# Optimization experiments

Measured on AMD Instinct MI355X. Metric: run time of the kernel, lower is better.

## Reference

```python
import jax, jax.numpy as jnp
import numpy as np

N = 20000
E = 320000
H = 16
C = 16
NUM_GRAPHS = 64
NEG_SLOPE = 0.2


def _gat(x, edge_index, W, a_src, a_dst, bias):
    # PyG GATConv, concat=True, shared lin for src/dst, eval mode (no dropout)
    h = (x @ W).reshape(-1, H, C)                       # [N,H,C]
    src, dst = edge_index[0], edge_index[1]
    alpha_src = jnp.sum(h * a_src, axis=-1)             # [N,H]
    alpha_dst = jnp.sum(h * a_dst, axis=-1)             # [N,H]
    alpha = alpha_src[src] + alpha_dst[dst]             # [E,H]
    alpha = jax.nn.leaky_relu(alpha, NEG_SLOPE)
    amax = jax.ops.segment_max(alpha, dst, num_segments=N)
    ex = jnp.exp(alpha - amax[dst])
    denom = jax.ops.segment_sum(ex, dst, num_segments=N)
    attn = ex / jnp.where(denom == 0, 1.0, denom)[dst]  # [E,H]
    msg = h[src] * attn[:, :, None]                     # [E,H,C]
    out = jax.ops.segment_sum(msg, dst, num_segments=N) # [N,H,C]
    return out.reshape(-1, H * C) + bias


def setup_inputs() -> dict:
    key = jax.random.key(0)
    ks = jax.random.split(key, 32)
    d = {}
    d['x'] = jax.random.normal(ks[0], (N, 20), dtype=jnp.float32)
    d['edge_index_ipv6'] = jax.random.randint(ks[1], (2, E), 0, N)
    d['edge_attr_ipv6'] = jax.random.normal(ks[2], (E, 19), dtype=jnp.float32)
    d['edge_index_tsch'] = jax.random.randint(ks[3], (2, E), 0, N)
    d['edge_attr_tsch'] = jax.random.normal(ks[4], (E, 7), dtype=jnp.float32)
    d['batch'] = jnp.sort(jax.random.randint(ks[5], (N,), 0, NUM_GRAPHS))
    s = 0.1
    d['W_i'] = jax.random.normal(ks[6], (20, H * C), dtype=jnp.float32) * s
    d['a_src_i'] = jax.random.normal(ks[7], (H, C), dtype=jnp.float32) * s
    d['a_dst_i'] = jax.random.normal(ks[8], (H, C), dtype=jnp.float32) * s
    d['b_i'] = jnp.zeros((H * C,), dtype=jnp.float32)
    d['W_t'] = jax.random.normal(ks[9], (20, H * C), dtype=jnp.float32) * s
    d['a_src_t'] = jax.random.normal(ks[10], (H, C), dtype=jnp.float32) * s
    d['a_dst_t'] = jax.random.normal(ks[11], (H, C), dtype=jnp.float32) * s
    d['b_t'] = jnp.zeros((H * C,), dtype=jnp.float32)
    d['Wf'] = jax.random.normal(ks[12], (512, 64), dtype=jnp.float32) * s
    d['bf'] = jnp.zeros((64,), dtype=jnp.float32)
    d['W1'] = jax.random.normal(ks[13], (64, 32), dtype=jnp.float32) * s
    d['b1'] = jnp.zeros((32,), dtype=jnp.float32)
    d['W2'] = jax.random.normal(ks[14], (32, 16), dtype=jnp.float32) * s
    d['b2'] = jnp.zeros((16,), dtype=jnp.float32)
    d['W3'] = jax.random.normal(ks[15], (16, 16), dtype=jnp.float32) * s
    d['b3'] = jnp.zeros((16,), dtype=jnp.float32)
    d['Wce'] = jax.random.normal(ks[16], (16, 3), dtype=jnp.float32) * s
    d['bce'] = jnp.zeros((3,), dtype=jnp.float32)
    d['Wcv'] = jax.random.normal(ks[17], (16, 3), dtype=jnp.float32) * s
    d['bcv'] = jnp.zeros((3,), dtype=jnp.float32)
    return d


def reference(x, edge_index_ipv6, edge_attr_ipv6, edge_index_tsch, edge_attr_tsch,
              batch, W_i, a_src_i, a_dst_i, b_i, W_t, a_src_t, a_dst_t, b_t,
              Wf, bf, W1, b1, W2, b2, W3, b3, Wce, bce, Wcv, bcv):
    # edge_attr_* are ignored by GATConv (edge_dim=None in PyG), as in original
    n_ipv6 = _gat(x, edge_index_ipv6, W_i, a_src_i, a_dst_i, b_i)
    n_tsch = _gat(x, edge_index_tsch, W_t, a_src_t, a_dst_t, b_t)
    h = jnp.concatenate([n_ipv6, n_tsch], axis=-1)      # [N,512]
    h = jax.nn.relu(h @ Wf + bf)
    h = jax.nn.relu(h @ W1 + b1)
    h = jax.nn.relu(h @ W2 + b2)
    h = jax.nn.relu(h @ W3 + b3)                        # [N,16]
    ssum = jax.ops.segment_sum(h, batch, num_segments=NUM_GRAPHS)
    cnt = jax.ops.segment_sum(jnp.ones((h.shape[0], 1), h.dtype), batch,
                              num_segments=NUM_GRAPHS)
    g = ssum / jnp.where(cnt == 0, 1.0, cnt)            # [G,16]
    out_event = g @ Wce + bce
    out_env = g @ Wcv + bcv
    return out_event, out_env
```

## Files before the change

### kernel.cpp

```cpp
#include <hip/hip_runtime.h>
#include <math.h>

#define N_NODES 20000
#define N_EDGES 320000
#define NG 64
#define NEG 0.2f
#define NCHUNK ((N_NODES + 255) / 256)
#define FLAGBIT (1 << 30)

typedef __attribute__((ext_vector_type(8))) short bf16x8;
typedef __attribute__((ext_vector_type(4))) float f32x4;

__device__ __forceinline__ unsigned short f2bf(float f) {
  unsigned int u = __float_as_uint(f);
  return (unsigned short)((u + 0x7fffu + ((u >> 16) & 1u)) >> 16);
}
__device__ __forceinline__ unsigned int pk2bf(float a, float b) {
  return (unsigned int)f2bf(a) | ((unsigned int)f2bf(b) << 16);
}

__global__ __launch_bounds__(256) void k_prep(
    const float* __restrict__ W_i, const float* __restrict__ as_i, const float* __restrict__ ad_i,
    const float* __restrict__ W_t, const float* __restrict__ as_t, const float* __restrict__ ad_t,
    const float* __restrict__ Wf, const float* __restrict__ bf,
    const float* __restrict__ b_i, const float* __restrict__ b_t,
    float* __restrict__ wsall, unsigned short* __restrict__ wbigfrag,
    float* __restrict__ bfold,
    int* __restrict__ fill_i, int* __restrict__ fill_t,
    float* __restrict__ gsum, int* __restrict__ gcnt, int* __restrict__ aggs) {
  __shared__ float bred[4][64];
  int idx = blockIdx.x * 256 + threadIdx.x;
  if (idx < 1280) {
    int k = idx >> 6, c = idx & 63;
    int set = c >> 5, role = (c >> 4) & 1, h = c & 15;
    const float* W = set ? W_t : W_i;
    const float* a = set ? (role ? ad_t : as_t) : (role ? ad_i : as_i);
    float v = 0.f;
#pragma unroll
    for (int j = 0; j < 16; ++j) v = fmaf(W[k * 256 + h * 16 + j], a[h * 16 + j], v);
    wsall[idx] = v;
    return;
  }
  idx -= 1280;
  if (idx < 40960) {
    int ct = idx / 10240, rem = idx % 10240;
    int lane = (rem >> 3) & 63, j = rem & 7, ks = rem >> 9;
    int k = ks * 32 + ((lane >> 4) << 3) + j;
    int nc = ct * 16 + (lane & 15);
    int g = (k >= 320) ? 1 : 0;
    int r = k - g * 320;
    int ch = r >> 4, h = r & 15;
    float v = 0.f;
    if (ch < 20) {
      const float* W = g ? W_t : W_i;
      const float* wr = W + ch * 256 + (h << 4);
      const float* wf = Wf + ((g << 8) + (h << 4)) * 64 + nc;
#pragma unroll
      for (int m = 0; m < 16; ++m) v = fmaf(wr[m], wf[m * 64], v);
    }
    wbigfrag[idx] = f2bf(v);
    return;
  }
  idx -= 40960;
  if (idx < 256) {
    int t = threadIdx.x, wv = t >> 6, j = t & 63;
    float p = 0.f;
    int i0 = wv * 128;
#pragma unroll 4
    for (int i = i0; i < i0 + 128; ++i) {
      float b = (i < 256) ? b_i[i] : b_t[i - 256];
      p = fmaf(b, Wf[i * 64 + j], p);
    }
    bred[wv][j] = p;
    __syncthreads();
    if (wv == 0) bfold[j] = bred[0][j] + bred[1][j] + bred[2][j] + bred[3][j] + bf[j];
    return;
  }
  idx -= 256;
  if (idx < N_NODES) { fill_i[idx] = 0; return; }
  idx -= N_NODES;
  if (idx < N_NODES) { fill_t[idx] = 0; return; }
  idx -= N_NODES;
  if (idx < NG * 16) { gsum[idx] = 0.f; return; }
  idx -= NG * 16;
  if (idx < NG) { gcnt[idx] = 0; return; }
  idx -= NG;
  if (idx < 256) aggs[idx] = 0;
}

__global__ __launch_bounds__(256) void k_alpha(
    const float* __restrict__ x, const float* __restrict__ wsall,
    unsigned short* __restrict__ xpadbf,
    float* __restrict__ asrc0, float* __restrict__ adst0,
    float* __restrict__ asrc1, float* __restrict__ adst1) {
  int t = threadIdx.x;
  int n0 = blockIdx.x * 16;
  __shared__ float xs[16][20];
  __shared__ float ws[20][64];
  for (int i = t; i < 16 * 20; i += 256) {
    int nd = i / 20, k = i % 20;
    xs[nd][k] = x[(n0 + nd) * 20 + k];
  }
  for (int i = t; i < 1280; i += 256) ws[i >> 6][i & 63] = wsall[i];
  __syncthreads();
  for (int i = t; i < 512; i += 256) {
    int nd = i >> 5, j = i & 31;
    float v = (j < 20) ? xs[nd][j] : (j == 20 ? 1.f : 0.f);
    xpadbf[(size_t)(n0 + nd) * 32 + j] = f2bf(v);
  }
#pragma unroll
  for (int i = 0; i < 4; ++i) {
    int wi = i * 256 + t;
    int nd = wi >> 6, c = wi & 63;
    float v = 0.f;
#pragma unroll
    for (int k = 0; k < 20; ++k) v = fmaf(xs[nd][k], ws[k][c], v);
    int n = n0 + nd, h = c & 15;
    float* arr = (c >> 5) ? ((c >> 4) & 1 ? adst1 : asrc1)
                          : ((c >> 4) & 1 ? adst0 : asrc0);
    arr[n * 16 + h] = v;
  }
}

__global__ void k_hist(const int* __restrict__ ei0, const int* __restrict__ ei1,
                       int* __restrict__ cnt0, int* __restrict__ cnt1) {
  int e = blockIdx.x * blockDim.x + threadIdx.x;
  if (e >= N_EDGES) return;
  if (blockIdx.y == 0)
    atomicAdd(&cnt0[ei0[N_EDGES + e]], 1);
  else
    atomicAdd(&cnt1[ei1[N_EDGES + e]], 1);
}

__global__ __launch_bounds__(256) void k_scan(
    int* __restrict__ fill0, int* __restrict__ fill1,
    int* __restrict__ rp0, int* __restrict__ rp1,
    int* __restrict__ aggs) {
  int chunk = blockIdx.x, set = blockIdx.y;
  int* fill = set ? fill1 : fill0;
  int* rp = set ? rp1 : rp0;
  int t = threadIdx.x, lane = t & 63, wv = t >> 6;
  int i = chunk * 256 + t;
  int v = (i < N_NODES) ? fill[i] : 0;
  int s = v;
#pragma unroll
  for (int d = 1; d < 64; d <<= 1) {
    int o = __shfl_up(s, d);
    if (lane >= d) s += o;
  }
  __shared__ int wsum[4];
  if (lane == 63) wsum[wv] = s;
  __syncthreads();
  int pre = 0;
#pragma unroll
  for (int j = 0; j < 4; ++j)
    if (j < wv) pre += wsum[j];
  s += pre;
  int agg = wsum[0] + wsum[1] + wsum[2] + wsum[3];
  if (t == 0)
    __hip_atomic_store(&aggs[set * 128 + chunk], agg | FLAGBIT,
                       __ATOMIC_RELEASE, __HIP_MEMORY_SCOPE_AGENT);
  __shared__ int reds[256];
  int part = 0;
  for (int j = t; j < chunk; j += 256) {
    int a;
    do {
      a = __hip_atomic_load(&aggs[set * 128 + j], __ATOMIC_ACQUIRE,
                            __HIP_MEMORY_SCOPE_AGENT);
    } while (!(a & FLAGBIT));
    part += a & (FLAGBIT - 1);
  }
  reds[t] = part;
  __syncthreads();
  for (int st = 128; st > 0; st >>= 1) {
    if (t < st) reds[t] += reds[t + st];
    __syncthreads();
  }
  int carry = reds[0];
  int excl = carry + s - v;
  if (i < N_NODES) {
    rp[i] = excl;
    fill[i] = excl;
    if (i == N_NODES - 1) rp[N_NODES] = excl + v;
  }
}

__global__ void k_scatter(const int* __restrict__ ei0, const int* __restrict__ ei1,
                          int* __restrict__ fill0, int* __restrict__ fill1,
                          unsigned short* __restrict__ srcs0,
                          unsigned short* __restrict__ srcs1) {
  int e = blockIdx.x * blockDim.x + threadIdx.x;
  if (e >= N_EDGES) return;
  const int* ei = blockIdx.y ? ei1 : ei0;
  int* fill = blockIdx.y ? fill1 : fill0;
  unsigned short* srcs = blockIdx.y ? srcs1 : srcs0;
  int d = ei[N_EDGES + e];
  int pos = atomicAdd(&fill[d], 1);
  srcs[pos] = (unsigned short)ei[e];
}

__global__ __launch_bounds__(256) void k_gat(
    const unsigned short* __restrict__ xpadbf,
    const float* __restrict__ asrc0, const float* __restrict__ adst0,
    const float* __restrict__ asrc1, const float* __restrict__ adst1,
    const int* __restrict__ rp0, const unsigned short* __restrict__ srcs0,
    const int* __restrict__ rp1, const unsigned short* __restrict__ srcs1,
    unsigned short* __restrict__ xagg) {
  __shared__ unsigned short exsh[4][16][40];
  __shared__ unsigned short xtsh[4][2][16][40];
  int w4 = threadIdx.x >> 6, lane = threadIdx.x & 63;
  int n = blockIdx.x * 2 + (w4 >> 1);
  int g = w4 & 1;
  int eid = lane & 15, slot = lane >> 4;
  unsigned short (*ext)[40] = exsh[w4];
  unsigned short (*xtw)[16][40] = xtsh[w4];
  const float* asrc = g ? asrc1 : asrc0;
  const float* adst = g ? adst1 : adst0;
  const int* rp = g ? rp1 : rp0;
  const unsigned short* srcs = g ? srcs1 : srcs0;
  int k0 = rp[n], k1 = rp[n + 1];
  const float4 adn4 = *(const float4*)&adst[n * 16 + slot * 4];
  f32x4 acc0 = {0.f, 0.f, 0.f, 0.f}, acc1 = acc0;
  int h16 = lane & 15, e8 = (lane >> 4) * 8;
  for (int base = k0; base < k1; base += 32) {
    int e0 = base + 2 * eid, e1 = e0 + 1;
    int sa = (int)srcs[min(e0, k1 - 1)];
    int sbb = (int)srcs[min(e1, k1 - 1)];
    const float4 ava = *(const float4*)&asrc[sa * 16 + slot * 4];
    const float4 avb = *(const float4*)&asrc[sbb * 16 + slot * 4];
    const uint4 xra = *(const uint4*)&xpadbf[(size_t)sa * 32 + slot * 8];
    const uint4 xrb = *(const uint4*)&xpadbf[(size_t)sbb * 32 + slot * 8];
    float ea[4], eb[4];
    {
      float a;
      bool v0 = e0 < k1, v1 = e1 < k1;
      a = ava.x + adn4.x; a = a >= 0.f ? a : NEG * a; ea[0] = v0 ? __expf(a) : 0.f;
      a = ava.y + adn4.y; a = a >= 0.f ? a : NEG * a; ea[1] = v0 ? __expf(a) : 0.f;
      a = ava.z + adn4.z; a = a >= 0.f ? a : NEG * a; ea[2] = v0 ? __expf(a) : 0.f;
      a = ava.w + adn4.w; a = a >= 0.f ? a : NEG * a; ea[3] = v0 ? __expf(a) : 0.f;
      a = avb.x + adn4.x; a = a >= 0.f ? a : NEG * a; eb[0] = v1 ? __expf(a) : 0.f;
      a = avb.y + adn4.y; a = a >= 0.f ? a : NEG * a; eb[1] = v1 ? __expf(a) : 0.f;
      a = avb.z + adn4.z; a = a >= 0.f ? a : NEG * a; eb[2] = v1 ? __expf(a) : 0.f;
      a = avb.w + adn4.w; a = a >= 0.f ? a : NEG * a; eb[3] = v1 ? __expf(a) : 0.f;
    }
#pragma unroll
    for (int r = 0; r < 4; ++r)
      *(unsigned int*)&ext[slot * 4 + r][2 * eid] = pk2bf(ea[r], eb[r]);
    unsigned int ua[4] = {xra.x, xra.y, xra.z, xra.w};
    unsigned int ub[4] = {xrb.x, xrb.y, xrb.z, xrb.w};
#pragma unroll
    for (int q = 0; q < 8; ++q) {
      unsigned int baq = (q & 1) ? (ua[q >> 1] >> 16) : (ua[q >> 1] & 0xffffu);
      unsigned int bbq = (q & 1) ? (ub[q >> 1] >> 16) : (ub[q >> 1] & 0xffffu);
      int ch = slot * 8 + q;
      *(unsigned int*)&xtw[ch >> 4][ch & 15][2 * eid] = baq | (bbq << 16);
    }
    bf16x8 A = *(const bf16x8*)&ext[h16][e8];
    bf16x8 B0 = *(const bf16x8*)&xtw[0][h16][e8];
    bf16x8 B1 = *(const bf16x8*)&xtw[1][h16][e8];
    acc0 = __builtin_amdgcn_mfma_f32_16x16x32_bf16(A, B0, acc0, 0, 0, 0);
    acc1 = __builtin_amdgcn_mfma_f32_16x16x32_bf16(A, B1, acc1, 0, 0, 0);
  }
  float inv[4];
#pragma unroll
  for (int r = 0; r < 4; ++r) {
    float dr = __shfl(acc1[r], (lane & 48) | 4);
    inv[r] = dr > 0.f ? 1.f / dr : 0.f;
  }
  int s = lane >> 4, c = lane & 15;
  size_t nb = (size_t)n * 640 + g * 320;
  uint2 o0;
  o0.x = pk2bf(acc0[0] * inv[0], acc0[1] * inv[1]);
  o0.y = pk2bf(acc0[2] * inv[2], acc0[3] * inv[3]);
  *(uint2*)&xagg[nb + c * 16 + s * 4] = o0;
  if (c < 4) {
    uint2 o1;
    o1.x = pk2bf(acc1[0] * inv[0], acc1[1] * inv[1]);
    o1.y = pk2bf(acc1[2] * inv[2], acc1[3] * inv[3]);
    *(uint2*)&xagg[nb + 256 + c * 16 + s * 4] = o1;
  }
}

__global__ __launch_bounds__(256) void k_mlp(
    const unsigned short* __restrict__ xagg, const unsigned short* __restrict__ wbigfrag,
    const float* __restrict__ bfold,
    const float* __restrict__ W1m, const float* __restrict__ b1v,
    const float* __restrict__ W2m, const float* __restrict__ b2v,
    const float* __restrict__ W3m, const float* __restrict__ b3v,
    const int* __restrict__ batch,
    float* __restrict__ gsum, int* __restrict__ gcnt) {
  int t = threadIdx.x, w = t >> 6, lane = t & 63;
  int n0 = blockIdx.x * 16;
  __shared__ float o1[16][68];
  __shared__ float o2[16][36];
  __shared__ float o3[16][20];
  __shared__ float o4[16][17];
  __shared__ int bs[16];
  if (t < 16) bs[t] = batch[n0 + t];

  {
    int m = lane & 15, kb = lane >> 4;
    const unsigned short* aptr = xagg + (size_t)(n0 + m) * 640 + kb * 8;
    const unsigned short* bbase = wbigfrag + (size_t)w * 10240 + lane * 8;
    f32x4 acc = {0.f, 0.f, 0.f, 0.f};
#pragma unroll 5
    for (int ks = 0; ks < 20; ++ks) {
      bf16x8 af = *(const bf16x8*)(aptr + ks * 32);
      bf16x8 bfr = *(const bf16x8*)(bbase + (size_t)ks * 512);
      acc = __builtin_amdgcn_mfma_f32_16x16x32_bf16(af, bfr, acc, 0, 0, 0);
    }
    int col = lane & 15, rg = lane >> 4;
#pragma unroll
    for (int r = 0; r < 4; ++r) {
      int row = rg * 4 + r;
      o1[row][w * 16 + col] = fmaxf(acc[r] + bfold[w * 16 + col], 0.f);
    }
  }
  __syncthreads();
  int nd = t >> 4, js = t & 15;
  {
    float a0 = b1v[js], a1 = b1v[js + 16];
#pragma unroll 8
    for (int k = 0; k < 64; ++k) {
      float hv = o1[nd][k];
      a0 = fmaf(hv, W1m[k * 32 + js], a0);
      a1 = fmaf(hv, W1m[k * 32 + js + 16], a1);
    }
    o2[nd][js] = fmaxf(a0, 0.f);
    o2[nd][js + 16] = fmaxf(a1, 0.f);
  }
  __syncthreads();
  {
    float a = b2v[js];
#pragma unroll
    for (int k = 0; k < 32; ++k) a = fmaf(o2[nd][k], W2m[k * 16 + js], a);
    o3[nd][js] = fmaxf(a, 0.f);
  }
  __syncthreads();
  {
    float a = b3v[js];
#pragma unroll
    for (int k = 0; k < 16; ++k) a = fmaf(o3[nd][k], W3m[k * 16 + js], a);
    o4[nd][js] = fmaxf(a, 0.f);
  }
  __syncthreads();
  if (t < 128) {
    int s = t >> 4, jx = t & 15;
    int b = bs[0] + s;
    if (b <= bs[15]) {
      float sum = 0.f; int c = 0;
#pragma unroll
      for (int ndd = 0; ndd < 16; ++ndd)
        if (bs[ndd] == b) { sum += o4[ndd][jx]; ++c; }
      if (c > 0) {
        atomicAdd(&gsum[b * 16 + jx], sum);
        if (jx == 0) atomicAdd(&gcnt[b], c);
      }
    }
  }
}

__global__ void k_head(const float* __restrict__ gsum, const int* __restrict__ gcnt,
                       const float* __restrict__ Wce, const float* __restrict__ bce,
                       const float* __restrict__ Wcv, const float* __restrict__ bcv,
                       float* __restrict__ out) {
  int t = threadIdx.x;
  if (t >= 384) return;
  int half = t / 192, idx = t % 192;
  int b = idx / 3, r = idx % 3;
  float cnt = (float)gcnt[b];
  float inv = cnt > 0.f ? 1.f / cnt : 1.f;
  const float* Wc = half ? Wcv : Wce;
  const float* bc = half ? bcv : bce;
  float v = bc[r];
#pragma unroll
  for (int j = 0; j < 16; ++j) v = fmaf(gsum[b * 16 + j] * inv, Wc[j * 3 + r], v);
  out[t] = v;
}

extern "C" void kernel_launch(void* const* d_in, const int* in_sizes, int n_in,
                              void* d_out, int out_size, void* d_ws, size_t ws_size,
                              hipStream_t stream) {
  const float* x = (const float*)d_in[0];
  const int* ei_i = (const int*)d_in[1];
  const int* ei_t = (const int*)d_in[3];
  const int* batch = (const int*)d_in[5];
  const float* W_i = (const float*)d_in[6];
  const float* as_i = (const float*)d_in[7];
  const float* ad_i = (const float*)d_in[8];
  const float* b_i = (const float*)d_in[9];
  const float* W_t = (const float*)d_in[10];
  const float* as_t = (const float*)d_in[11];
  const float* ad_t = (const float*)d_in[12];
  const float* b_t = (const float*)d_in[13];
  const float* Wf = (const float*)d_in[14];
  const float* bf = (const float*)d_in[15];
  const float* W1 = (const float*)d_in[16];
  const float* b1 = (const float*)d_in[17];
  const float* W2 = (const float*)d_in[18];
  const float* b2 = (const float*)d_in[19];
  const float* W3 = (const float*)d_in[20];
  const float* b3 = (const float*)d_in[21];
  const float* Wce = (const float*)d_in[22];
  const float* bce = (const float*)d_in[23];
  const float* Wcv = (const float*)d_in[24];
  const float* bcv = (const float*)d_in[25];

  char* ws = (char*)d_ws;
  size_t off = 0;
  auto take = [&](size_t bytes) {
    void* p = ws + off;
    off = (off + bytes + 255) & ~(size_t)255;
    return p;
  };
  unsigned short* xpadbf = (unsigned short*)take((size_t)N_NODES * 32 * 2);
  unsigned short* xagg = (unsigned short*)take((size_t)N_NODES * 640 * 2);
  float* wsall = (float*)take((size_t)1280 * 4);
  unsigned short* wbigfrag = (unsigned short*)take((size_t)40960 * 2);
  float* bfold = (float*)take((size_t)64 * 4);
  float* asrc_i = (float*)take((size_t)N_NODES * 16 * 4);
  float* adst_i = (float*)take((size_t)N_NODES * 16 * 4);
  float* asrc_t = (float*)take((size_t)N_NODES * 16 * 4);
  float* adst_t = (float*)take((size_t)N_NODES * 16 * 4);
  int* rowptr_i = (int*)take((size_t)(N_NODES + 1) * 4);
  int* rowptr_t = (int*)take((size_t)(N_NODES + 1) * 4);
  int* fill_i = (int*)take((size_t)N_NODES * 4);
  int* fill_t = (int*)take((size_t)N_NODES * 4);
  int* csums = (int*)take((size_t)2 * 128 * 4);
  unsigned short* srcs_i = (unsigned short*)take((size_t)N_EDGES * 2);
  unsigned short* srcs_t = (unsigned short*)take((size_t)N_EDGES * 2);
  float* gsum = (float*)take((size_t)NG * 16 * 4);
  int* gcnt = (int*)take((size_t)NG * 4);

  int prep_items = 1280 + 40960 + 256 + N_NODES + N_NODES + NG * 16 + NG + 256;
  k_prep<<<(prep_items + 255) / 256, 256, 0, stream>>>(
      W_i, as_i, ad_i, W_t, as_t, ad_t, Wf, bf, b_i, b_t,
      wsall, wbigfrag, bfold, fill_i, fill_t, gsum, gcnt, csums);

  k_alpha<<<N_NODES / 16, 256, 0, stream>>>(x, wsall, xpadbf,
                                            asrc_i, adst_i, asrc_t, adst_t);

  dim3 egrid((N_EDGES + 255) / 256, 2);
  k_hist<<<egrid, 256, 0, stream>>>(ei_i, ei_t, fill_i, fill_t);
  dim3 sgrid(NCHUNK, 2);
  k_scan<<<sgrid, 256, 0, stream>>>(fill_i, fill_t, rowptr_i, rowptr_t, csums);
  k_scatter<<<egrid, 256, 0, stream>>>(ei_i, ei_t, fill_i, fill_t, srcs_i, srcs_t);

  k_gat<<<N_NODES / 2, 256, 0, stream>>>(xpadbf, asrc_i, adst_i, asrc_t, adst_t,
                                         rowptr_i, srcs_i, rowptr_t, srcs_t,
                                         xagg);

  k_mlp<<<N_NODES / 16, 256, 0, stream>>>(xagg, wbigfrag, bfold,
                                          W1, b1, W2, b2, W3, b3,
                                          batch, gsum, gcnt);

  k_head<<<1, 384, 0, stream>>>(gsum, gcnt, Wce, bce, Wcv, bcv, (float*)d_out);
}
```

Baseline: 136.8 us.

## Fuse prep, alpha and histogram kernels into one front kernel; zero buffers via memset

Merges the weight-prep, per-node attention-logit, and in-degree histogram kernels into a single launch. Each node-block now recomputes the folded W·a weights in shared memory instead of reading a precomputed buffer, and also handles 256 edges of the histogram for both graphs. Buffer zeroing moves to two hipMemsetAsync calls over contiguous allocations. The aim is fewer launches and fewer inter-kernel dependencies, at the cost of redundant weight folding in every block and memsets that still serialize on the stream.

```diff
diff --git a/kernel.cpp b/kernel.cpp
--- a/kernel.cpp
+++ b/kernel.cpp
@@ -19,30 +19,24 @@
   return (unsigned int)f2bf(a) | ((unsigned int)f2bf(b) << 16);
 }
 
-__global__ __launch_bounds__(256) void k_prep(
+__global__ __launch_bounds__(256) void k_front(
+    const float* __restrict__ x,
     const float* __restrict__ W_i, const float* __restrict__ as_i, const float* __restrict__ ad_i,
     const float* __restrict__ W_t, const float* __restrict__ as_t, const float* __restrict__ ad_t,
     const float* __restrict__ Wf, const float* __restrict__ bf,
     const float* __restrict__ b_i, const float* __restrict__ b_t,
-    float* __restrict__ wsall, unsigned short* __restrict__ wbigfrag,
-    float* __restrict__ bfold,
-    int* __restrict__ fill_i, int* __restrict__ fill_t,
-    float* __restrict__ gsum, int* __restrict__ gcnt, int* __restrict__ aggs) {
+    const int* __restrict__ ei0, const int* __restrict__ ei1,
+    unsigned short* __restrict__ wbigfrag, float* __restrict__ bfold,
+    unsigned short* __restrict__ xpadbf,
+    float* __restrict__ asrc0, float* __restrict__ adst0,
+    float* __restrict__ asrc1, float* __restrict__ adst1,
+    int* __restrict__ fill0, int* __restrict__ fill1) {
   __shared__ float bred[4][64];
-  int idx = blockIdx.x * 256 + threadIdx.x;
-  if (idx < 1280) {
-    int k = idx >> 6, c = idx & 63;
-    int set = c >> 5, role = (c >> 4) & 1, h = c & 15;
-    const float* W = set ? W_t : W_i;
-    const float* a = set ? (role ? ad_t : as_t) : (role ? ad_i : as_i);
-    float v = 0.f;
-#pragma unroll
-    for (int j = 0; j < 16; ++j) v = fmaf(W[k * 256 + h * 16 + j], a[h * 16 + j], v);
-    wsall[idx] = v;
-    return;
-  }
-  idx -= 1280;
-  if (idx < 40960) {
+  __shared__ float xs[16][20];
+  __shared__ float ws[20][64];
+  int b = blockIdx.x, t = threadIdx.x;
+  if (b < 160) {
+    int idx = b * 256 + t;
     int ct = idx / 10240, rem = idx % 10240;
     int lane = (rem >> 3) & 63, j = rem & 7, ks = rem >> 9;
     int k = ks * 32 + ((lane >> 4) << 3) + j;
@@ -61,47 +55,41 @@
     wbigfrag[idx] = f2bf(v);
     return;
   }
-  idx -= 40960;
-  if (idx < 256) {
-    int t = threadIdx.x, wv = t >> 6, j = t & 63;
+  if (b == 160) {
+    int wv = t >> 6, j = t & 63;
     float p = 0.f;
     int i0 = wv * 128;
 #pragma unroll 4
     for (int i = i0; i < i0 + 128; ++i) {
-      float b = (i < 256) ? b_i[i] : b_t[i - 256];
-      p = fmaf(b, Wf[i * 64 + j], p);
+      float bb = (i < 256) ? b_i[i] : b_t[i - 256];
+      p = fmaf(bb, Wf[i * 64 + j], p);
     }
     bred[wv][j] = p;
     __syncthreads();
     if (wv == 0) bfold[j] = bred[0][j] + bred[1][j] + bred[2][j] + bred[3][j] + bf[j];
     return;
   }
-  idx -= 256;
-  if (idx < N_NODES) { fill_i[idx] = 0; return; }
-  idx -= N_NODES;
-  if (idx < N_NODES) { fill_t[idx] = 0; return; }
-  idx -= N_NODES;
-  if (idx < NG * 16) { gsum[idx] = 0.f; return; }
-  idx -= NG * 16;
-  if (idx < NG) { gcnt[idx] = 0; return; }
-  idx -= NG;
-  if (idx < 256) aggs[idx] = 0;
-}
-
-__global__ __launch_bounds__(256) void k_alpha(
-    const float* __restrict__ x, const float* __restrict__ wsall,
-    unsigned short* __restrict__ xpadbf,
-    float* __restrict__ asrc0, float* __restrict__ adst0,
-    float* __restrict__ asrc1, float* __restrict__ adst1) {
-  int t = threadIdx.x;
-  int n0 = blockIdx.x * 16;
-  __shared__ float xs[16][20];
-  __shared__ float ws[20][64];
-  for (int i = t; i < 16 * 20; i += 256) {
+  int a = b - 161;
+  int e = a * 256 + t;
+  int d0 = ei0[N_EDGES + e];
+  int d1 = ei1[N_EDGES + e];
+  atomicAdd(&fill0[d0], 1);
+  atomicAdd(&fill1[d1], 1);
+  int n0 = a * 16;
+  for (int i = t; i < 320; i += 256) {
     int nd = i / 20, k = i % 20;
     xs[nd][k] = x[(n0 + nd) * 20 + k];
   }
-  for (int i = t; i < 1280; i += 256) ws[i >> 6][i & 63] = wsall[i];
+  for (int i = t; i < 1280; i += 256) {
+    int k = i >> 6, c = i & 63;
+    int set = c >> 5, role = (c >> 4) & 1, h = c & 15;
+    const float* W = set ? W_t : W_i;
+    const float* av = set ? (role ? ad_t : as_t) : (role ? ad_i : as_i);
+    float v = 0.f;
+#pragma unroll
+    for (int j = 0; j < 16; ++j) v = fmaf(W[k * 256 + h * 16 + j], av[h * 16 + j], v);
+    ws[k][c] = v;
+  }
   __syncthreads();
   for (int i = t; i < 512; i += 256) {
     int nd = i >> 5, j = i & 31;
@@ -120,16 +108,6 @@
                           : ((c >> 4) & 1 ? adst0 : asrc0);
     arr[n * 16 + h] = v;
   }
-}
-
-__global__ void k_hist(const int* __restrict__ ei0, const int* __restrict__ ei1,
-                       int* __restrict__ cnt0, int* __restrict__ cnt1) {
-  int e = blockIdx.x * blockDim.x + threadIdx.x;
-  if (e >= N_EDGES) return;
-  if (blockIdx.y == 0)
-    atomicAdd(&cnt0[ei0[N_EDGES + e]], 1);
-  else
-    atomicAdd(&cnt1[ei1[N_EDGES + e]], 1);
 }
 
 __global__ __launch_bounds__(256) void k_scan(
@@ -415,7 +393,6 @@
   };
   unsigned short* xpadbf = (unsigned short*)take((size_t)N_NODES * 32 * 2);
   unsigned short* xagg = (unsigned short*)take((size_t)N_NODES * 640 * 2);
-  float* wsall = (float*)take((size_t)1280 * 4);
   unsigned short* wbigfrag = (unsigned short*)take((size_t)40960 * 2);
   float* bfold = (float*)take((size_t)64 * 4);
   float* asrc_i = (float*)take((size_t)N_NODES * 16 * 4);
@@ -424,26 +401,27 @@
   float* adst_t = (float*)take((size_t)N_NODES * 16 * 4);
   int* rowptr_i = (int*)take((size_t)(N_NODES + 1) * 4);
   int* rowptr_t = (int*)take((size_t)(N_NODES + 1) * 4);
-  int* fill_i = (int*)take((size_t)N_NODES * 4);
-  int* fill_t = (int*)take((size_t)N_NODES * 4);
-  int* csums = (int*)take((size_t)2 * 128 * 4);
+  int* fill_i = (int*)take((size_t)2 * N_NODES * 4);
+  int* fill_t = fill_i + N_NODES;
   unsigned short* srcs_i = (unsigned short*)take((size_t)N_EDGES * 2);
   unsigned short* srcs_t = (unsigned short*)take((size_t)N_EDGES * 2);
-  float* gsum = (float*)take((size_t)NG * 16 * 4);
-  int* gcnt = (int*)take((size_t)NG * 4);
-
-  int prep_items = 1280 + 40960 + 256 + N_NODES + N_NODES + NG * 16 + NG + 256;
-  k_prep<<<(prep_items + 255) / 256, 256, 0, stream>>>(
-      W_i, as_i, ad_i, W_t, as_t, ad_t, Wf, bf, b_i, b_t,
-      wsall, wbigfrag, bfold, fill_i, fill_t, gsum, gcnt, csums);
-
-  k_alpha<<<N_NODES / 16, 256, 0, stream>>>(x, wsall, xpadbf,
-                                            asrc_i, adst_i, asrc_t, adst_t);
-
-  dim3 egrid((N_EDGES + 255) / 256, 2);
-  k_hist<<<egrid, 256, 0, stream>>>(ei_i, ei_t, fill_i, fill_t);
+  float* gsum = (float*)take((size_t)(NG * 16 + NG + 256) * 4);
+  int* gcnt = (int*)(gsum + NG * 16);
+  int* csums = gcnt + NG;
+
+  hipMemsetAsync(fill_i, 0, (size_t)2 * N_NODES * 4, stream);
+  hipMemsetAsync(gsum, 0, (size_t)(NG * 16 + NG + 256) * 4, stream);
+
+  k_front<<<1411, 256, 0, stream>>>(x, W_i, as_i, ad_i, W_t, as_t, ad_t,
+                                    Wf, bf, b_i, b_t, ei_i, ei_t,
+                                    wbigfrag, bfold, xpadbf,
+                                    asrc_i, adst_i, asrc_t, adst_t,
+                                    fill_i, fill_t);
+
   dim3 sgrid(NCHUNK, 2);
   k_scan<<<sgrid, 256, 0, stream>>>(fill_i, fill_t, rowptr_i, rowptr_t, csums);
+
+  dim3 egrid((N_EDGES + 255) / 256, 2);
   k_scatter<<<egrid, 256, 0, stream>>>(ei_i, ei_t, fill_i, fill_t, srcs_i, srcs_t);
 
   k_gat<<<N_NODES / 2, 256, 0, stream>>>(xpadbf, asrc_i, adst_i, asrc_t, adst_t,
```

Result: no change. 137.8 us (+0.7%).
